# Performance work log

Hardware: AMD Instinct MI355X
Metric: run time of the kernel (lower is better)

Reference implementation:

```python
import jax, jax.numpy as jnp
import numpy as np

NUM_GROUPS = 2048  # ix values drawn from [0, NUM_GROUPS); stands in for torch.unique's group count

def setup_inputs() -> dict:
    key = jax.random.key(0)
    ks = jax.random.split(key, 9)
    B, E, D = 2, 32768, 512
    s = 1.0 / np.sqrt(D)  # nn.Linear default init scale
    x = jax.random.normal(ks[0], (B, E, D), jnp.float32)
    ix = jax.random.randint(ks[1], (E,), 0, NUM_GROUPS)
    Wf = jax.random.uniform(ks[2], (D, D), jnp.float32, -s, s)
    bf = jax.random.uniform(ks[3], (D,), jnp.float32, -s, s)
    Wg = jax.random.uniform(ks[4], (D, D), jnp.float32, -s, s)
    bg = jax.random.uniform(ks[5], (D,), jnp.float32, -s, s)
    Wh = jax.random.uniform(ks[6], (D, D), jnp.float32, -s, s)
    bh = jax.random.uniform(ks[7], (D,), jnp.float32, -s, s)
    return {"x": x, "ix": ix, "Wf": Wf, "bf": bf, "Wg": Wg, "bg": bg, "Wh": Wh, "bh": bh}

def reference(x, ix, Wf, bf, Wg, bg, Wh, bh):
    # Linear projections (nn.Linear: x @ W.T + b)
    logits = jnp.einsum('bed,kd->bek', x, Wg) + bg  # g(x): (B,E,D)
    vals   = jnp.einsum('bed,kd->bek', x, Wf) + bf  # f(x): (B,E,D)
    # Move edges to leading axis for segment ops: (E,B,D)
    lt = jnp.transpose(logits, (1, 0, 2))
    vt = jnp.transpose(vals, (1, 0, 2))
    # Group-wise (scatter) softmax over edges sharing the same ix
    m = jax.ops.segment_max(lt, ix, num_segments=NUM_GROUPS)      # (G,B,D)
    e = jnp.exp(lt - m[ix])                                        # (E,B,D)
    denom = jax.ops.segment_sum(e, ix, num_segments=NUM_GROUPS)   # (G,B,D)
    w = e / denom[ix]                                              # (E,B,D)
    # Weighted scatter-sum per group
    y = jax.ops.segment_sum(vt * w, ix, num_segments=NUM_GROUPS)  # (G,B,D)
    y = jnp.transpose(y, (1, 0, 2))                                # (B,G,D)
    out = jnp.einsum('bgd,kd->bgk', y, Wh) + bh                    # h(y)
    return out[:, ix]                                              # expand back to (B,E,D)
```

## Files before the change

### kernel.cpp

```cpp
#include <hip/hip_runtime.h>
#include <hip/hip_bf16.h>
#include <cstdint>
#include <cstddef>

typedef __bf16 bf16x8 __attribute__((ext_vector_type(8)));
typedef float f32x4 __attribute__((ext_vector_type(4)));
using u16 = unsigned short;

#define NUM_GROUPS_C 2048

__device__ __forceinline__ u16 f2bf(float f) {
  union { float f; uint32_t u; } c; c.f = f;
  uint32_t r = (c.u + 0x7fffu + ((c.u >> 16) & 1u)) >> 16;
  return (u16)r;
}
__device__ __forceinline__ float bf2f(u16 h) {
  union { uint32_t u; float f; } c; c.u = ((uint32_t)h) << 16; return c.f;
}

__device__ __forceinline__ void glds16(const u16* g, void* l) {
  __builtin_amdgcn_global_load_lds((const __attribute__((address_space(1))) void*)g,
                                   (__attribute__((address_space(3))) void*)l, 16, 0, 0);
}

__global__ void cast_f32_bf16(const float* __restrict__ src, u16* __restrict__ dst, long n4) {
  long i = (long)blockIdx.x * blockDim.x + threadIdx.x;
  long stride = (long)gridDim.x * blockDim.x;
  for (; i < n4; i += stride) {
    float4 v = reinterpret_cast<const float4*>(src)[i];
    uint2 o;
    o.x = (uint32_t)f2bf(v.x) | ((uint32_t)f2bf(v.y) << 16);
    o.y = (uint32_t)f2bf(v.z) | ((uint32_t)f2bf(v.w) << 16);
    reinterpret_cast<uint2*>(dst)[i] = o;
  }
}

__global__ void cast_w3(const float* __restrict__ w0, const float* __restrict__ w1,
                        const float* __restrict__ w2,
                        u16* __restrict__ o0, u16* __restrict__ o1, u16* __restrict__ o2,
                        int n4) {
  const float* src = (blockIdx.y == 0) ? w0 : (blockIdx.y == 1) ? w1 : w2;
  u16* dst = (blockIdx.y == 0) ? o0 : (blockIdx.y == 1) ? o1 : o2;
  int i = blockIdx.x * blockDim.x + threadIdx.x;
  int stride = gridDim.x * blockDim.x;
  for (; i < n4; i += stride) {
    float4 v = reinterpret_cast<const float4*>(src)[i];
    uint2 o;
    o.x = (uint32_t)f2bf(v.x) | ((uint32_t)f2bf(v.y) << 16);
    o.y = (uint32_t)f2bf(v.z) | ((uint32_t)f2bf(v.w) << 16);
    reinterpret_cast<uint2*>(dst)[i] = o;
  }
}

__global__ void zero_i32(int* p, int n) {
  int i = blockIdx.x * blockDim.x + threadIdx.x;
  if (i < n) p[i] = 0;
}
__global__ void count_k(const int* __restrict__ ix, int* __restrict__ cnt, int E) {
  int e = blockIdx.x * blockDim.x + threadIdx.x;
  if (e < E) atomicAdd(&cnt[ix[e]], 1);
}
__global__ void scan_k(const int* __restrict__ cnt, int* __restrict__ offs,
                       int* __restrict__ cursor, int G) {
  __shared__ int part[256];
  int t = threadIdx.x;
  int gpt = G / 256;
  int base = t * gpt;
  int loc[8];
  int s = 0;
  for (int j = 0; j < gpt; ++j) { loc[j] = cnt[base + j]; s += loc[j]; }
  part[t] = s;
  __syncthreads();
  for (int off = 1; off < 256; off <<= 1) {
    int v = (t >= off) ? part[t - off] : 0;
    __syncthreads();
    part[t] += v;
    __syncthreads();
  }
  int run = part[t] - s;
  for (int j = 0; j < gpt; ++j) {
    offs[base + j] = run;
    cursor[base + j] = run;
    run += loc[j];
  }
}
__global__ void scatter_k(const int* __restrict__ ix, int* __restrict__ cursor,
                          int* __restrict__ elist, int E) {
  int e = blockIdx.x * blockDim.x + threadIdx.x;
  if (e < E) {
    int g = ix[e];
    int pos = atomicAdd(&cursor[g], 1);
    elist[pos] = e;
  }
}

__global__ __launch_bounds__(512, 2)
void gemm256_pl(const u16* __restrict__ A,
                const u16* __restrict__ B0g, const u16* __restrict__ B1g,
                const float* __restrict__ bias0, const float* __restrict__ bias1,
                u16* __restrict__ C0, u16* __restrict__ C1,
                int K, int N) {
  __shared__ u16 lds[65536];

  const int tid  = threadIdx.x;
  const int lane = tid & 63;
  const int wid  = tid >> 6;
  const int wm   = wid >> 2;
  const int wn   = wid & 3;
  const int fr   = lane & 15;
  const int fq   = lane >> 4;
  const int swr  = fr & 7;

  const int nwg = gridDim.x, cpx = nwg >> 3, wg = blockIdx.x;
  const int swz = (wg & 7) * cpx + (wg >> 3);
  const int mt = swz >> 2, ns = swz & 3;
  const u16* Bm     = (ns < 2) ? B0g : B1g;
  const float* bias = (ns < 2) ? bias0 : bias1;
  u16* C            = (ns < 2) ? C0 : C1;
  const int n0 = (ns & 1) * 256, m0 = mt * 256;

  const int r8   = tid >> 3;
  const int scol = ((tid & 7) ^ (r8 & 7)) << 3;
  const u16* Ab = A  + (size_t)m0 * K + scol;
  const u16* Bb = Bm + (size_t)n0 * K + scol;
  char* ldsb = (char*)lds;

  auto stage_ht = [&](int p, int isB, int h, int kt) {
    const u16* src = (isB ? Bb : Ab) + (size_t)(h * 128 + r8) * K + kt * 64;
    char* dst = ldsb + p * 65536 + isB * 32768 + h * 16384 + wid * 1024;
    glds16(src, dst);
    glds16(src + (size_t)64 * K, dst + 8192);
  };

#define RD4_A(dst, base, mio)                                                       \
  _Pragma("unroll") for (int j = 0; j < 4; ++j)                                     \
  _Pragma("unroll") for (int kk = 0; kk < 2; ++kk)                                  \
    dst[j][kk] = *(const bf16x8*)((base) + ((((mio) + j) * 32 + wm * 16 + fr) << 7) \
                                         + ((((kk << 2) | fq) ^ swr) << 4));
#define RD2_B(dst, base, njo)                                                       \
  _Pragma("unroll") for (int j = 0; j < 2; ++j)                                     \
  _Pragma("unroll") for (int kk = 0; kk < 2; ++kk)                                  \
    dst[j][kk] = *(const bf16x8*)((base) + ((((njo) + j) * 64 + wn * 16 + fr) << 7) \
                                         + ((((kk << 2) | fq) ^ swr) << 4));
#define MFMA_Q(accm, accn, af, bf_)                                                \
  __builtin_amdgcn_s_setprio(1);                                                  \
  _Pragma("unroll") for (int j = 0; j < 4; ++j)                                    \
  _Pragma("unroll") for (int jn = 0; jn < 2; ++jn)                                 \
  _Pragma("unroll") for (int kk = 0; kk < 2; ++kk)                                 \
    acc[(accm) + j][(accn) + jn] = __builtin_amdgcn_mfma_f32_16x16x32_bf16(        \
        af[j][kk], bf_[jn][kk], acc[(accm) + j][(accn) + jn], 0, 0, 0);            \
  __builtin_amdgcn_s_setprio(0);

  f32x4 acc[8][4] = {};
  bf16x8 a0[4][2], a1[4][2], b0[2][2], b1[2][2];
  const int NT = K >> 6;

  stage_ht(0, 1, 0, 0);
  stage_ht(0, 0, 0, 0);
  stage_ht(0, 1, 1, 0);
  stage_ht(0, 0, 1, 0);
  asm volatile("s_waitcnt vmcnt(0)" ::: "memory");
  __builtin_amdgcn_s_barrier();
  RD4_A(a0, ldsb, 0)

#define KT_BODY(cb_, kt_)                                                          \
  {                                                                                \
    const int nb_ = (cb_) ^ 1;                                                     \
    const int ks_ = ((kt_) + 1 < NT) ? (kt_) + 1 : NT - 1;                         \
    const char* sA_ = ldsb + (cb_) * 65536;                                        \
    const char* sB_ = sA_ + 32768;                                                 \
    const char* nA_ = ldsb + nb_ * 65536;                                          \
                                                                          \
    RD2_B(b0, sB_, 0)                                                              \
    RD2_B(b1, sB_, 2)                                                              \
    MFMA_Q(0, 0, a0, b0)                                                           \
    stage_ht(nb_, 1, 0, ks_);                                                      \
    asm volatile("s_waitcnt vmcnt(2)" ::: "memory");                               \
    __builtin_amdgcn_s_barrier();                                                  \
                                                                          \
    RD4_A(a1, sA_, 4)                                                              \
    MFMA_Q(0, 2, a0, b1)                                                           \
    stage_ht(nb_, 0, 0, ks_);                                                      \
    __builtin_amdgcn_s_barrier();                                                  \
                                                                          \
    MFMA_Q(4, 2, a1, b1)                                                           \
    stage_ht(nb_, 1, 1, ks_);                                                      \
    asm volatile("s_waitcnt vmcnt(2)" ::: "memory");                               \
    __builtin_amdgcn_s_barrier();                                                  \
           \
    RD4_A(a0, nA_, 0)                                                              \
    MFMA_Q(4, 0, a1, b0)                                                           \
    stage_ht(nb_, 0, 1, ks_);                                                      \
    asm volatile("s_waitcnt vmcnt(2)" ::: "memory");                               \
    __builtin_amdgcn_s_barrier();                                                  \
  }

  for (int kt = 0; kt < NT; kt += 2) {
    KT_BODY(0, kt)
    KT_BODY(1, kt + 1)
  }
  asm volatile("s_waitcnt vmcnt(0)" ::: "memory");

#undef KT_BODY
#undef RD4_A
#undef RD2_B
#undef MFMA_Q

  #pragma unroll
  for (int mi = 0; mi < 8; ++mi) {
    const int row = m0 + mi * 32 + wm * 16 + fq * 4;
    #pragma unroll
    for (int ni = 0; ni < 4; ++ni) {
      const int col = n0 + ni * 64 + wn * 16 + fr;
      const float bvv = bias[col];
      #pragma unroll
      for (int r = 0; r < 4; ++r)
        C[(size_t)(row + r) * N + col] = f2bf(acc[mi][ni][r] + bvv);
    }
  }
}

__device__ __forceinline__ void stage_tile_128x64(const u16* __restrict__ src, int ld,
                                                  u16* lds, int tid) {
  int wid = tid >> 6;
  #pragma unroll
  for (int i = 0; i < 4; ++i) {
    int c = i * 256 + tid;
    const u16* g = src + (size_t)(c >> 3) * ld + ((c & 7) << 3);
    char* l = (char*)lds + ((i * 4 + wid) << 10);
    glds16(g, l);
  }
}

__global__ __launch_bounds__(256)
void gemm_bf16_nt_f32out(const u16* __restrict__ A, const u16* __restrict__ Bm,
                         const float* __restrict__ bias,
                         float* __restrict__ C, int K, int N) {
  __shared__ u16 sA[128 * 64];
  __shared__ u16 sB[128 * 64];

  int tid = threadIdx.x;
  const int m0 = blockIdx.x * 128, n0 = blockIdx.y * 128;
  const u16* Ap = A + (size_t)m0 * K;
  const u16* Bp = Bm + (size_t)n0 * K;

  int lane = tid & 63;
  int wid = tid >> 6;
  int wm = wid >> 1, wn = wid & 1;
  int fr = lane & 15;
  int fq = lane >> 4;

  f32x4 acc[4][4] = {};

  for (int k0 = 0; k0 < K; k0 += 64) {
    stage_tile_128x64(Ap + k0, K, sA, tid);
    stage_tile_128x64(Bp + k0, K, sB, tid);
    __syncthreads();
    #pragma unroll
    for (int kk = 0; kk < 2; ++kk) {
      bf16x8 af[4], bfrag[4];
      #pragma unroll
      for (int mi = 0; mi < 4; ++mi)
        af[mi] = *reinterpret_cast<const bf16x8*>(&sA[(wm * 64 + mi * 16 + fr) * 64 + kk * 32 + fq * 8]);
      #pragma unroll
      for (int nj = 0; nj < 4; ++nj)
        bfrag[nj] = *reinterpret_cast<const bf16x8*>(&sB[(wn * 64 + nj * 16 + fr) * 64 + kk * 32 + fq * 8]);
      #pragma unroll
      for (int mi = 0; mi < 4; ++mi)
        #pragma unroll
        for (int nj = 0; nj < 4; ++nj)
          acc[mi][nj] = __builtin_amdgcn_mfma_f32_16x16x32_bf16(af[mi], bfrag[nj], acc[mi][nj], 0, 0, 0);
    }
    __syncthreads();
  }

  #pragma unroll
  for (int nj = 0; nj < 4; ++nj) {
    int col = n0 + wn * 64 + nj * 16 + fr;
    float bv = bias[col];
    #pragma unroll
    for (int mi = 0; mi < 4; ++mi) {
      int rowb = m0 + wm * 64 + mi * 16 + fq * 4;
      #pragma unroll
      for (int r = 0; r < 4; ++r)
        C[(size_t)(rowb + r) * N + col] = acc[mi][nj][r] + bv;
    }
  }
}

__global__ __launch_bounds__(256)
void seg_softmax(const u16* __restrict__ lg, const u16* __restrict__ vl,
                 const int* __restrict__ cnt, const int* __restrict__ offs,
                 const int* __restrict__ elist,
                 u16* __restrict__ y, int E, int D, int B, int G) {
  __shared__ int eids[256];
  int g = blockIdx.x / B;
  int b = blockIdx.x - g * B;
  int t = threadIdx.x;
  int n = cnt[g], start = offs[g];
  int d0 = t * 2;

  float m0 = -1e30f, m1 = -1e30f, s0 = 0.f, s1 = 0.f, a0 = 0.f, a1 = 0.f;
  for (int c0 = 0; c0 < n; c0 += 256) {
    int nc = n - c0; if (nc > 256) nc = 256;
    __syncthreads();
    if (t < nc) eids[t] = elist[start + c0 + t];
    __syncthreads();
    for (int i = 0; i < nc; ++i) {
      size_t base = ((size_t)b * E + eids[i]) * D + d0;
      uint32_t lu = *reinterpret_cast<const uint32_t*>(lg + base);
      uint32_t vu = *reinterpret_cast<const uint32_t*>(vl + base);
      float l0 = bf2f((u16)(lu & 0xffffu)), l1 = bf2f((u16)(lu >> 16));
      float v0 = bf2f((u16)(vu & 0xffffu)), v1 = bf2f((u16)(vu >> 16));
      float nm0 = fmaxf(m0, l0);
      float sc0 = __expf(m0 - nm0), w0 = __expf(l0 - nm0);
      s0 = s0 * sc0 + w0; a0 = a0 * sc0 + w0 * v0; m0 = nm0;
      float nm1 = fmaxf(m1, l1);
      float sc1 = __expf(m1 - nm1), w1 = __expf(l1 - nm1);
      s1 = s1 * sc1 + w1; a1 = a1 * sc1 + w1 * v1; m1 = nm1;
    }
  }
  float r0 = (n > 0) ? a0 / s0 : 0.f;
  float r1 = (n > 0) ? a1 / s1 : 0.f;
  size_t yoff = ((size_t)b * G + g) * D + d0;
  uint32_t o = (uint32_t)f2bf(r0) | ((uint32_t)f2bf(r1) << 16);
  *reinterpret_cast<uint32_t*>(y + yoff) = o;
}

__global__ void gather_k(const float* __restrict__ of, const int* __restrict__ ix,
                         float* __restrict__ out, int E, int D, int G) {
  int be = blockIdx.x;
  int b = be / E;
  int e = be - b * E;
  int gsel = ix[e];
  const float4* src = reinterpret_cast<const float4*>(of + ((size_t)b * G + gsel) * D);
  float4* dst = reinterpret_cast<float4*>(out + (size_t)be * D);
  for (int t = threadIdx.x; t < D / 4; t += blockDim.x)
    dst[t] = src[t];
}

extern "C" void kernel_launch(void* const* d_in, const int* in_sizes, int n_in,
                              void* d_out, int out_size, void* d_ws, size_t ws_size,
                              hipStream_t stream) {
  const float* x   = (const float*)d_in[0];
  const int*   ix  = (const int*)d_in[1];
  const float* Wf  = (const float*)d_in[2];
  const float* bfb = (const float*)d_in[3];
  const float* Wg  = (const float*)d_in[4];
  const float* bg  = (const float*)d_in[5];
  const float* Wh  = (const float*)d_in[6];
  const float* bh  = (const float*)d_in[7];

  const int E = in_sizes[1];
  const int D = in_sizes[3];
  const int B = in_sizes[0] / (E * D);
  const int G = NUM_GROUPS_C;
  const int M = B * E;
  const long xn = (long)M * D;

  char* ws = (char*)d_ws;
  size_t off = 0;
  auto alloc = [&](size_t bytes) -> char* {
    char* p = ws + off;
    off += (bytes + 255) & ~(size_t)255;
    return p;
  };
  u16* xb  = (u16*)alloc((size_t)M * D * 2);
  u16* lgb = (u16*)alloc((size_t)M * D * 2);
  u16* vlb = (u16*)alloc((size_t)M * D * 2);
  u16* Wgb = (u16*)alloc((size_t)D * D * 2);
  u16* Wfb = (u16*)alloc((size_t)D * D * 2);
  u16* Whb = (u16*)alloc((size_t)D * D * 2);
  u16* yb  = (u16*)alloc((size_t)B * G * D * 2);
  float* ofb = (float*)alloc((size_t)B * G * D * 4);
  int* cnt    = (int*)alloc((size_t)G * 4);
  int* offs   = (int*)alloc((size_t)G * 4);
  int* cursor = (int*)alloc((size_t)G * 4);
  int* elist  = (int*)alloc((size_t)E * 4);

  cast_f32_bf16<<<2048, 256, 0, stream>>>(x, xb, xn / 4);
  dim3 gw(64, 3);
  cast_w3<<<gw, 256, 0, stream>>>(Wg, Wf, Wh, Wgb, Wfb, Whb, D * D / 4);

  zero_i32<<<(G + 255) / 256, 256, 0, stream>>>(cnt, G);
  count_k<<<(E + 255) / 256, 256, 0, stream>>>(ix, cnt, E);
  scan_k<<<1, 256, 0, stream>>>(cnt, offs, cursor, G);
  scatter_k<<<(E + 255) / 256, 256, 0, stream>>>(ix, cursor, elist, E);

  gemm256_pl<<<(M / 256) * 4, 512, 0, stream>>>(xb, Wgb, Wfb, bg, bfb, lgb, vlb, D, D);

  seg_softmax<<<G * B, 256, 0, stream>>>(lgb, vlb, cnt, offs, elist, yb, E, D, B, G);

  dim3 gh((B * G) / 128, D / 128);
  gemm_bf16_nt_f32out<<<gh, 256, 0, stream>>>(yb, Whb, bh, ofb, D, D);

  gather_k<<<B * E, 128, 0, stream>>>(ofb, ix, (float*)d_out, E, D, G);
}
```

Before: 225.9 us.

## Deepen GEMM pipeline with register double-buffering and two-tile-ahead LDS staging

After: 307.0 us. 35.9% more time.

```diff
diff --git a/kernel.cpp b/kernel.cpp
--- a/kernel.cpp
+++ b/kernel.cpp
@@ -95,7 +95,7 @@
 }
 
 __global__ __launch_bounds__(512, 2)
-void gemm256_pl(const u16* __restrict__ A,
+void gemm256_dp(const u16* __restrict__ A,
                 const u16* __restrict__ B0g, const u16* __restrict__ B1g,
                 const float* __restrict__ bias0, const float* __restrict__ bias1,
                 u16* __restrict__ C0, u16* __restrict__ C1,
@@ -152,52 +152,62 @@
   __builtin_amdgcn_s_setprio(0);
 
   f32x4 acc[8][4] = {};
-  bf16x8 a0[4][2], a1[4][2], b0[2][2], b1[2][2];
+  bf16x8 a0A[4][2], a0B[4][2], a1[4][2];
+  bf16x8 b0A[2][2], b0B[2][2], b1A[2][2], b1B[2][2];
   const int NT = K >> 6;
 
   stage_ht(0, 1, 0, 0);
   stage_ht(0, 0, 0, 0);
   stage_ht(0, 1, 1, 0);
   stage_ht(0, 0, 1, 0);
+  stage_ht(1, 1, 0, 1);
   asm volatile("s_waitcnt vmcnt(0)" ::: "memory");
   __builtin_amdgcn_s_barrier();
-  RD4_A(a0, ldsb, 0)
-
-#define KT_BODY(cb_, kt_)                                                          \
+  {
+    const char* pA = ldsb;
+    const char* pB = ldsb + 32768;
+    RD4_A(a0A, pA, 0)
+    RD2_B(b0A, pB, 0)
+    RD2_B(b1A, pB, 2)
+  }
+  stage_ht(1, 1, 1, 1);
+  stage_ht(1, 0, 0, 1);
+
+#define KT_BODY(cb_, kt_, a0c, b0c, b1c, a0n, b0n, b1n)                            \
   {                                                                                \
     const int nb_ = (cb_) ^ 1;                                                     \
-    const int ks_ = ((kt_) + 1 < NT) ? (kt_) + 1 : NT - 1;                         \
-    const char* sA_ = ldsb + (cb_) * 65536;                                        \
-    const char* sB_ = sA_ + 32768;                                                 \
-    const char* nA_ = ldsb + nb_ * 65536;                                          \
+    const int ks1 = ((kt_) + 1 < NT) ? (kt_) + 1 : NT - 1;                         \
+    const int ks2 = ((kt_) + 2 < NT) ? (kt_) + 2 : NT - 1;                         \
+    const char* cA = ldsb + (cb_) * 65536;                                         \
+    const char* nA = ldsb + nb_ * 65536;                                           \
+    const char* nB = nA + 32768;                                                   \
                                                                           \
-    RD2_B(b0, sB_, 0)                                                              \
-    RD2_B(b1, sB_, 2)                                                              \
-    MFMA_Q(0, 0, a0, b0)                                                           \
-    stage_ht(nb_, 1, 0, ks_);                                                      \
-    asm volatile("s_waitcnt vmcnt(2)" ::: "memory");                               \
+    RD2_B(b0n, nB, 0)                                                              \
+    MFMA_Q(0, 0, a0c, b0c)                                                         \
+    stage_ht(nb_, 0, 1, ks1);                                                      \
     __builtin_amdgcn_s_barrier();                                                  \
                                                                           \
-    RD4_A(a1, sA_, 4)                                                              \
-    MFMA_Q(0, 2, a0, b1)                                                           \
-    stage_ht(nb_, 0, 0, ks_);                                                      \
+    RD4_A(a1, cA, 4)                                                               \
+    MFMA_Q(0, 2, a0c, b1c)                                                         \
+    stage_ht(cb_, 1, 0, ks2);                                                      \
+    asm volatile("s_waitcnt vmcnt(4)" ::: "memory");                               \
     __builtin_amdgcn_s_barrier();                                                  \
                                                                           \
-    MFMA_Q(4, 2, a1, b1)                                                           \
-    stage_ht(nb_, 1, 1, ks_);                                                      \
-    asm volatile("s_waitcnt vmcnt(2)" ::: "memory");                               \
+    RD2_B(b1n, nB, 2)                                                              \
+    MFMA_Q(4, 2, a1, b1c)                                                          \
+    stage_ht(cb_, 1, 1, ks2);                                                      \
     __builtin_amdgcn_s_barrier();                                                  \
-           \
-    RD4_A(a0, nA_, 0)                                                              \
-    MFMA_Q(4, 0, a1, b0)                                                           \
-    stage_ht(nb_, 0, 1, ks_);                                                      \
-    asm volatile("s_waitcnt vmcnt(2)" ::: "memory");                               \
+                                                                          \
+    RD4_A(a0n, nA, 0)                                                              \
+    MFMA_Q(4, 0, a1, b0c)                                                          \
+    stage_ht(cb_, 0, 0, ks2);                                                      \
+    asm volatile("s_waitcnt vmcnt(4)" ::: "memory");                               \
     __builtin_amdgcn_s_barrier();                                                  \
   }
 
   for (int kt = 0; kt < NT; kt += 2) {
-    KT_BODY(0, kt)
-    KT_BODY(1, kt + 1)
+    KT_BODY(0, kt,     a0A, b0A, b1A, a0B, b0B, b1B)
+    KT_BODY(1, kt + 1, a0B, b0B, b1B, a0A, b0A, b1A)
   }
   asm volatile("s_waitcnt vmcnt(0)" ::: "memory");
 
@@ -387,7 +397,7 @@
   scan_k<<<1, 256, 0, stream>>>(cnt, offs, cursor, G);
   scatter_k<<<(E + 255) / 256, 256, 0, stream>>>(ix, cursor, elist, E);
 
-  gemm256_pl<<<(M / 256) * 4, 512, 0, stream>>>(xb, Wgb, Wfb, bg, bfb, lgb, vlb, D, D);
+  gemm256_dp<<<(M / 256) * 4, 512, 0, stream>>>(xb, Wgb, Wfb, bg, bfb, lgb, vlb, D, D);
 
   seg_softmax<<<G * B, 256, 0, stream>>>(lgb, vlb, cnt, offs, elist, yb, E, D, B, G);
 
```
